# Optimization experiments

Hardware: AMD Instinct MI355X
Metric: run time of the kernel (lower is better)

The kernel has to match this reference:

```python
import jax, jax.numpy as jnp
import numpy as np


def setup_inputs() -> dict:
    key = jax.random.key(0)
    k1, k2 = jax.random.split(key)
    B, S, D = 4, 8192, 2048
    FO, K = 2, 3
    x = jax.random.normal(k1, (B, S, D), dtype=jnp.float32)
    filters = jax.random.normal(k2, (FO, B, S, K), dtype=jnp.float32)
    return {"x": x, "filters": filters}


def reference(x, filters):
    """Gated depthwise causal conv (Hyena mixing op), causal=True path.

    Per-order kernel = mean over seq dim of filters[i] -> (B, K), shared across
    all d_model channels. PyTorch F.conv1d is cross-correlation with
    padding=K-1 then slice to seq_len, i.e. out[b,t,c] = sum_j k[b,j] * x[b, t+j-(K-1), c].
    Orders are summed (linear), so we sum kernels first and do one pass.
    """
    B, S, D = x.shape
    K = filters.shape[-1]
    # mean over seq_len, then sum over filter_order -> (B, K)
    k = filters.mean(axis=2).sum(axis=0)
    # flip so out[b,t,c] = sum_j kf[b,j] * x[b, t-j, c] (causal)
    kf = k[:, ::-1]
    xp = jnp.pad(x, ((0, 0), (K - 1, 0), (0, 0)))  # (B, S+K-1, D)
    out = jnp.zeros_like(x)
    for j in range(K):  # K is tiny (3); static unrolled loop
        out = out + kf[:, j][:, None, None] * jax.lax.dynamic_slice_in_dim(xp, K - 1 - j, S, axis=1)
    return out
```

## Files before the change

kernel.cpp:

```cpp
#include <hip/hip_runtime.h>


constexpr int B_ = 4;
constexpr int S_ = 8192;
constexpr int D_ = 2048;
constexpr int K_ = 3;
constexpr int TC = 32;
constexpr int LD4 = D_ / 4;

typedef float f4 __attribute__((ext_vector_type(4)));

__global__ __launch_bounds__(256) void reduce_partial_kernel(
    const float* __restrict__ filters, float* __restrict__ partials) {
    const int bid   = blockIdx.x;
    const int tid   = threadIdx.x;
    const int fo    = bid >> 5;
    const int b     = (bid >> 3) & 3;
    const int slice = bid & 7;

    const f4* F = (const f4*)filters;
    const int base_f4 = (fo * 4 + b) * 6144 + slice * 768;

    const f4 a  = F[base_f4 + 3 * tid + 0];
    const f4 bb = F[base_f4 + 3 * tid + 1];
    const f4 c  = F[base_f4 + 3 * tid + 2];

    float s0 = a.x + a.w + bb.z + c.y;
    float s1 = a.y + bb.x + bb.w + c.z;
    float s2 = a.z + bb.y + c.x + c.w;

    __shared__ float red[3][256];
    red[0][tid] = s0; red[1][tid] = s1; red[2][tid] = s2;
    __syncthreads();
    for (int off = 128; off > 0; off >>= 1) {
        if (tid < off) {
            red[0][tid] += red[0][tid + off];
            red[1][tid] += red[1][tid + off];
            red[2][tid] += red[2][tid + off];
        }
        __syncthreads();
    }
    if (tid < 3) partials[bid * 3 + tid] = red[tid][0];
}

__global__ __launch_bounds__(256) void causal_conv_kernel(
    const float* __restrict__ x, const float* __restrict__ partials,
    float* __restrict__ out) {
    const int bid    = blockIdx.x;
    const int tid    = threadIdx.x;
    const int nchunk = S_ / TC;
    const int tchunk = bid % nchunk;
    const int b      = bid / nchunk;
    const int t0     = tchunk * TC;

    __shared__ float ksh[3];
    if (tid < 3) {
        float s = 0.f;
        #pragma unroll
        for (int fo = 0; fo < 2; ++fo)
            #pragma unroll
            for (int sl = 0; sl < 8; ++sl)
                s += partials[(fo * 32 + b * 8 + sl) * 3 + tid];
        ksh[tid] = s * (1.0f / (float)S_);
    }
    __syncthreads();
    const float k0 = ksh[0], k1 = ksh[1], k2 = ksh[2];

    const f4* xb = (const f4*)x + (size_t)b * S_ * LD4;
    f4*       ob = (f4*)out     + (size_t)b * S_ * LD4;
    const int ca = tid;
    const int cb = tid + 256;

    f4 z = (f4)(0.f);
    f4 am2 = (t0 >= 2) ? xb[(size_t)(t0 - 2) * LD4 + ca] : z;
    f4 am1 = (t0 >= 1) ? xb[(size_t)(t0 - 1) * LD4 + ca] : z;
    f4 bm2 = (t0 >= 2) ? xb[(size_t)(t0 - 2) * LD4 + cb] : z;
    f4 bm1 = (t0 >= 1) ? xb[(size_t)(t0 - 1) * LD4 + cb] : z;

    #pragma unroll
    for (int g = 0; g < TC / 4; ++g) {
        f4 xa[4], xv[4];
        #pragma unroll
        for (int u = 0; u < 4; ++u) {
            const size_t t = (size_t)(t0 + g * 4 + u);
            xa[u] = xb[t * LD4 + ca];
            xv[u] = xb[t * LD4 + cb];
        }
        #pragma unroll
        for (int u = 0; u < 4; ++u) {
            const size_t t = (size_t)(t0 + g * 4 + u);
            f4 oa = k2 * xa[u] + k1 * am1 + k0 * am2;
            f4 ov = k2 * xv[u] + k1 * bm1 + k0 * bm2;
            __builtin_nontemporal_store(oa, &ob[t * LD4 + ca]);
            __builtin_nontemporal_store(ov, &ob[t * LD4 + cb]);
            am2 = am1; am1 = xa[u];
            bm2 = bm1; bm1 = xv[u];
        }
    }
}

extern "C" void kernel_launch(void* const* d_in, const int* in_sizes, int n_in,
                              void* d_out, int out_size, void* d_ws, size_t ws_size,
                              hipStream_t stream) {
    const float* x        = (const float*)d_in[0];
    const float* filters  = (const float*)d_in[1];
    float*       out      = (float*)d_out;
    float*       partials = (float*)d_ws;

    reduce_partial_kernel<<<64, 256, 0, stream>>>(filters, partials);

    const int nblocks = B_ * (S_ / TC);
    causal_conv_kernel<<<nblocks, 256, 0, stream>>>(x, partials, out);
}
```

Before: 93.84 us.

## Fuse filter reduction into conv kernel with atomic flag handoff

Merges the filter-mean reduction kernel into the causal conv kernel. The first 64 blocks compute the partial sums, now reduced with wavefront shuffles instead of a shared-memory tree, and signal completion through a global atomic counter. Every block issues its halo loads before spin-waiting on that counter, which hides the reduction behind x loads and removes one kernel launch gap. In exchange it adds a memset launch and spin-wait synchronisation that depends on the first 64 blocks being scheduled early, which risks deadlock if they are not.

```diff
diff --git a/kernel.cpp b/kernel.cpp
--- a/kernel.cpp
+++ b/kernel.cpp
@@ -4,54 +4,78 @@
 constexpr int B_ = 4;
 constexpr int S_ = 8192;
 constexpr int D_ = 2048;
-constexpr int K_ = 3;
 constexpr int TC = 32;
 constexpr int LD4 = D_ / 4;
 
 typedef float f4 __attribute__((ext_vector_type(4)));
 
-__global__ __launch_bounds__(256) void reduce_partial_kernel(
-    const float* __restrict__ filters, float* __restrict__ partials) {
-    const int bid   = blockIdx.x;
-    const int tid   = threadIdx.x;
-    const int fo    = bid >> 5;
-    const int b     = (bid >> 3) & 3;
-    const int slice = bid & 7;
+__global__ __launch_bounds__(256) void fused_conv_kernel(
+    const float* __restrict__ x, const float* __restrict__ filters,
+    float* __restrict__ out, float* __restrict__ partials,
+    unsigned* __restrict__ flag) {
+    const int bid = blockIdx.x;
+    const int tid = threadIdx.x;
 
-    const f4* F = (const f4*)filters;
-    const int base_f4 = (fo * 4 + b) * 6144 + slice * 768;
+    if (bid < 64) {
+        const int fo    = bid >> 5;
+        const int fb    = (bid >> 3) & 3;
+        const int slice = bid & 7;
+        const f4* F = (const f4*)filters;
+        const int base_f4 = (fo * 4 + fb) * 6144 + slice * 768;
 
-    const f4 a  = F[base_f4 + 3 * tid + 0];
-    const f4 bb = F[base_f4 + 3 * tid + 1];
-    const f4 c  = F[base_f4 + 3 * tid + 2];
+        const f4 a  = F[base_f4 + 3 * tid + 0];
+        const f4 bb = F[base_f4 + 3 * tid + 1];
+        const f4 c  = F[base_f4 + 3 * tid + 2];
 
-    float s0 = a.x + a.w + bb.z + c.y;
-    float s1 = a.y + bb.x + bb.w + c.z;
-    float s2 = a.z + bb.y + c.x + c.w;
+        float s0 = a.x + a.w + bb.z + c.y;
+        float s1 = a.y + bb.x + bb.w + c.z;
+        float s2 = a.z + bb.y + c.x + c.w;
 
-    __shared__ float red[3][256];
-    red[0][tid] = s0; red[1][tid] = s1; red[2][tid] = s2;
-    __syncthreads();
-    for (int off = 128; off > 0; off >>= 1) {
-        if (tid < off) {
-            red[0][tid] += red[0][tid + off];
-            red[1][tid] += red[1][tid + off];
-            red[2][tid] += red[2][tid + off];
+        #pragma unroll
+        for (int off = 32; off > 0; off >>= 1) {
+            s0 += __shfl_xor(s0, off);
+            s1 += __shfl_xor(s1, off);
+            s2 += __shfl_xor(s2, off);
+        }
+        __shared__ float wred[4][3];
+        const int wv = tid >> 6;
+        if ((tid & 63) == 0) {
+            wred[wv][0] = s0; wred[wv][1] = s1; wred[wv][2] = s2;
         }
         __syncthreads();
+        if (tid < 3) {
+            partials[bid * 3 + tid] =
+                wred[0][tid] + wred[1][tid] + wred[2][tid] + wred[3][tid];
+            __threadfence();
+        }
+        __syncthreads();
+        if (tid == 0)
+            __hip_atomic_fetch_add(flag, 1u, __ATOMIC_RELEASE,
+                                   __HIP_MEMORY_SCOPE_AGENT);
     }
-    if (tid < 3) partials[bid * 3 + tid] = red[tid][0];
-}
 
-__global__ __launch_bounds__(256) void causal_conv_kernel(
-    const float* __restrict__ x, const float* __restrict__ partials,
-    float* __restrict__ out) {
-    const int bid    = blockIdx.x;
-    const int tid    = threadIdx.x;
     const int nchunk = S_ / TC;
     const int tchunk = bid % nchunk;
     const int b      = bid / nchunk;
     const int t0     = tchunk * TC;
+
+    const f4* xb = (const f4*)x + (size_t)b * S_ * LD4;
+    f4*       ob = (f4*)out     + (size_t)b * S_ * LD4;
+    const int ca = tid;
+    const int cb = tid + 256;
+
+    f4 z = (f4)(0.f);
+    f4 am2 = (t0 >= 2) ? xb[(size_t)(t0 - 2) * LD4 + ca] : z;
+    f4 am1 = (t0 >= 1) ? xb[(size_t)(t0 - 1) * LD4 + ca] : z;
+    f4 bm2 = (t0 >= 2) ? xb[(size_t)(t0 - 2) * LD4 + cb] : z;
+    f4 bm1 = (t0 >= 1) ? xb[(size_t)(t0 - 1) * LD4 + cb] : z;
+
+    if (tid == 0) {
+        while (__hip_atomic_load(flag, __ATOMIC_ACQUIRE,
+                                 __HIP_MEMORY_SCOPE_AGENT) < 64u)
+            __builtin_amdgcn_s_sleep(2);
+    }
+    __syncthreads();
 
     __shared__ float ksh[3];
     if (tid < 3) {
@@ -65,17 +89,6 @@
     }
     __syncthreads();
     const float k0 = ksh[0], k1 = ksh[1], k2 = ksh[2];
-
-    const f4* xb = (const f4*)x + (size_t)b * S_ * LD4;
-    f4*       ob = (f4*)out     + (size_t)b * S_ * LD4;
-    const int ca = tid;
-    const int cb = tid + 256;
-
-    f4 z = (f4)(0.f);
-    f4 am2 = (t0 >= 2) ? xb[(size_t)(t0 - 2) * LD4 + ca] : z;
-    f4 am1 = (t0 >= 1) ? xb[(size_t)(t0 - 1) * LD4 + ca] : z;
-    f4 bm2 = (t0 >= 2) ? xb[(size_t)(t0 - 2) * LD4 + cb] : z;
-    f4 bm1 = (t0 >= 1) ? xb[(size_t)(t0 - 1) * LD4 + cb] : z;
 
     #pragma unroll
     for (int g = 0; g < TC / 4; ++g) {
@@ -102,13 +115,15 @@
 extern "C" void kernel_launch(void* const* d_in, const int* in_sizes, int n_in,
                               void* d_out, int out_size, void* d_ws, size_t ws_size,
                               hipStream_t stream) {
-    const float* x        = (const float*)d_in[0];
-    const float* filters  = (const float*)d_in[1];
-    float*       out      = (float*)d_out;
+    const float* x       = (const float*)d_in[0];
+    const float* filters = (const float*)d_in[1];
+    float*       out     = (float*)d_out;
     float*       partials = (float*)d_ws;
+    unsigned*    flag     = (unsigned*)((char*)d_ws + 1024);
 
-    reduce_partial_kernel<<<64, 256, 0, stream>>>(filters, partials);
+    hipMemsetAsync(flag, 0, sizeof(unsigned), stream);
 
     const int nblocks = B_ * (S_ / TC);
-    causal_conv_kernel<<<nblocks, 256, 0, stream>>>(x, partials, out);
+    fused_conv_kernel<<<nblocks, 256, 0, stream>>>(x, filters, out,
+                                                   partials, flag);
 }
```

New measurement: 124.6 us. +32.8%, slower.
